# Kernel optimization log

Measured on AMD Instinct MI355X. Metric: run time of the kernel, lower is better.

## Reference

```python
import jax, jax.numpy as jnp
import numpy as np


def setup_inputs() -> dict:
    key = jax.random.key(0)
    k1, k2 = jax.random.split(key)
    quantum_state = jax.random.normal(k1, (8, 2048, 1024), dtype=jnp.float32)
    gate_params = jax.random.normal(k2, (3, 10, 4), dtype=jnp.float32)  # (n_layers, n_qubits, 4)
    return {"quantum_state": quantum_state, "gate_params": gate_params}


def _total_factor(gate_params):
    # gate.sum() = cos(a)e^{ib} + sin(a)e^{ig} - sin(a)e^{-ig} + cos(a)e^{-ib}
    #            = 2*cos(a)*cos(b) + 2j*sin(a)*sin(g)   (delta unused)
    a = gate_params[..., 0]
    b = gate_params[..., 1]
    g = gate_params[..., 2]
    re = 2.0 * jnp.cos(a) * jnp.cos(b)
    im = 2.0 * jnp.sin(a) * jnp.sin(g)
    s = jax.lax.complex(re, im).astype(jnp.complex64)  # (3, n_qubits)
    return jnp.prod(s)  # single complex scalar


def reference(quantum_state, gate_params):
    factor = _total_factor(gate_params)
    # torch: real state * complex scalar -> complex64 output
    return quantum_state.astype(jnp.complex64) * factor
```

## Files before the change

### kernel.cpp

```cpp
#include <hip/hip_runtime.h>


typedef float fvec4 __attribute__((ext_vector_type(4)));

__device__ __forceinline__ float2 wave_factor(const float* __restrict__ gp) {
    const int lane = threadIdx.x & 63;
    float re = 1.0f, im = 0.0f;
    if (lane < 30) {
        const float a = gp[lane * 4 + 0];
        const float b = gp[lane * 4 + 1];
        const float g = gp[lane * 4 + 2];
        re = 2.0f * cosf(a) * cosf(b);
        im = 2.0f * sinf(a) * sinf(g);
    }
    #pragma unroll
    for (int m = 1; m < 64; m <<= 1) {
        const float ore = __shfl_xor(re, m, 64);
        const float oim = __shfl_xor(im, m, 64);
        const float nre = re * ore - im * oim;
        const float nim = re * oim + im * ore;
        re = nre;
        im = nim;
    }
    return make_float2(re, im);
}

__global__ void __launch_bounds__(256) qp_real_kernel(const float* __restrict__ state,
                                                      const float* __restrict__ gp,
                                                      float* __restrict__ out,
                                                      long long n4 ) {
    const float fr = wave_factor(gp).x;
    const fvec4* __restrict__ in4 = reinterpret_cast<const fvec4*>(state);
    fvec4* __restrict__ out4 = reinterpret_cast<fvec4*>(out);
    const long long stride = (long long)gridDim.x * blockDim.x;
    for (long long i = (long long)blockIdx.x * blockDim.x + threadIdx.x; i < n4; i += stride) {
        fvec4 s = in4[i];
        fvec4 o = s * fr;
        __builtin_nontemporal_store(o, &out4[i]);
    }
}

__global__ void __launch_bounds__(256) qp_complex_kernel(const float* __restrict__ state,
                                                         const float* __restrict__ gp,
                                                         float* __restrict__ out,
                                                         long long n2 ) {
    const float2 f = wave_factor(gp);
    const float fr = f.x, fi = f.y;
    const float2* __restrict__ in2 = reinterpret_cast<const float2*>(state);
    fvec4* __restrict__ out4 = reinterpret_cast<fvec4*>(out);
    const long long stride = (long long)gridDim.x * blockDim.x;
    for (long long i = (long long)blockIdx.x * blockDim.x + threadIdx.x; i < n2; i += stride) {
        float2 s = in2[i];
        fvec4 o;
        o.x = s.x * fr;
        o.y = s.x * fi;
        o.z = s.y * fr;
        o.w = s.y * fi;
        __builtin_nontemporal_store(o, &out4[i]);
    }
}

extern "C" void kernel_launch(void* const* d_in, const int* in_sizes, int n_in,
                              void* d_out, int out_size, void* d_ws, size_t ws_size,
                              hipStream_t stream) {
    const float* state = (const float*)d_in[0];
    const float* gp = (const float*)d_in[1];
    float* out = (float*)d_out;

    const long long N = (long long)in_sizes[0];

    const int block = 256;
    const int grid = 4096;

    if ((long long)out_size == 2 * N) {
        qp_complex_kernel<<<grid, block, 0, stream>>>(state, gp, out, N / 2);
    } else {
        qp_real_kernel<<<grid, block, 0, stream>>>(state, gp, out, N / 4);
    }
}
```

Measured before the change: 25.83 us.

## Prefetch next state element, overlap factor computation with load, halve grid

Each kernel now issues its first state load before computing the gate factor, so memory latency overlaps the trig and shuffle reduction. The grid-stride loop is software-pipelined to load the next element before storing the current one. Fast __sinf/__cosf intrinsics replace the precise versions, nontemporal stores become regular stores, and the grid drops from 4096 to 2048 blocks. The fast intrinsics lower accuracy of the factor, and dropping nontemporal stores may change cache behaviour for the large output.

```diff
diff --git a/kernel.cpp b/kernel.cpp
--- a/kernel.cpp
+++ b/kernel.cpp
@@ -10,8 +10,8 @@
         const float a = gp[lane * 4 + 0];
         const float b = gp[lane * 4 + 1];
         const float g = gp[lane * 4 + 2];
-        re = 2.0f * cosf(a) * cosf(b);
-        im = 2.0f * sinf(a) * sinf(g);
+        re = 2.0f * __cosf(a) * __cosf(b);
+        im = 2.0f * __sinf(a) * __sinf(g);
     }
     #pragma unroll
     for (int m = 1; m < 64; m <<= 1) {
@@ -29,35 +29,55 @@
                                                       const float* __restrict__ gp,
                                                       float* __restrict__ out,
                                                       long long n4 ) {
-    const float fr = wave_factor(gp).x;
     const fvec4* __restrict__ in4 = reinterpret_cast<const fvec4*>(state);
     fvec4* __restrict__ out4 = reinterpret_cast<fvec4*>(out);
     const long long stride = (long long)gridDim.x * blockDim.x;
-    for (long long i = (long long)blockIdx.x * blockDim.x + threadIdx.x; i < n4; i += stride) {
-        fvec4 s = in4[i];
-        fvec4 o = s * fr;
-        __builtin_nontemporal_store(o, &out4[i]);
+    long long i = (long long)blockIdx.x * blockDim.x + threadIdx.x;
+    if (i >= n4) return;
+
+    fvec4 s = in4[i];
+    const float fr = wave_factor(gp).x;
+
+    while (i + stride < n4) {
+        fvec4 nxt = in4[i + stride];
+        out4[i] = s * fr;
+        s = nxt;
+        i += stride;
     }
+    out4[i] = s * fr;
 }
 
 __global__ void __launch_bounds__(256) qp_complex_kernel(const float* __restrict__ state,
                                                          const float* __restrict__ gp,
                                                          float* __restrict__ out,
                                                          long long n2 ) {
-    const float2 f = wave_factor(gp);
-    const float fr = f.x, fi = f.y;
     const float2* __restrict__ in2 = reinterpret_cast<const float2*>(state);
     fvec4* __restrict__ out4 = reinterpret_cast<fvec4*>(out);
     const long long stride = (long long)gridDim.x * blockDim.x;
-    for (long long i = (long long)blockIdx.x * blockDim.x + threadIdx.x; i < n2; i += stride) {
-        float2 s = in2[i];
+    long long i = (long long)blockIdx.x * blockDim.x + threadIdx.x;
+    if (i >= n2) return;
+
+    float2 s = in2[i];
+    const float2 f = wave_factor(gp);
+    const float fr = f.x, fi = f.y;
+
+    while (i + stride < n2) {
+        float2 nxt = in2[i + stride];
         fvec4 o;
         o.x = s.x * fr;
         o.y = s.x * fi;
         o.z = s.y * fr;
         o.w = s.y * fi;
-        __builtin_nontemporal_store(o, &out4[i]);
+        out4[i] = o;
+        s = nxt;
+        i += stride;
     }
+    fvec4 o;
+    o.x = s.x * fr;
+    o.y = s.x * fi;
+    o.z = s.y * fr;
+    o.w = s.y * fi;
+    out4[i] = o;
 }
 
 extern "C" void kernel_launch(void* const* d_in, const int* in_sizes, int n_in,
@@ -70,7 +90,7 @@
     const long long N = (long long)in_sizes[0];
 
     const int block = 256;
-    const int grid = 4096;
+    const int grid = 2048;
 
     if ((long long)out_size == 2 * N) {
         qp_complex_kernel<<<grid, block, 0, stream>>>(state, gp, out, N / 2);
```

Result: no change. 25.98 us (+0.6%).

## Launch one thread per element, drop grid-stride loop, use fast trig intrinsics

Applied to the files above, without the earlier changes.

Replaces the fixed 4096-block grid-stride loop with a grid sized to the data, so each thread processes a single element. The input load is issued before the factor reduction so the two can overlap. Trig calls are switched to the fast intrinsics and plain stores replace the nontemporal ones. The cost is that every thread recomputes the wave-level factor reduction once per element, and the fast intrinsics give slightly less accurate sine and cosine values.

```diff
diff --git a/kernel.cpp b/kernel.cpp
--- a/kernel.cpp
+++ b/kernel.cpp
@@ -10,8 +10,8 @@
         const float a = gp[lane * 4 + 0];
         const float b = gp[lane * 4 + 1];
         const float g = gp[lane * 4 + 2];
-        re = 2.0f * cosf(a) * cosf(b);
-        im = 2.0f * sinf(a) * sinf(g);
+        re = 2.0f * __cosf(a) * __cosf(b);
+        im = 2.0f * __sinf(a) * __sinf(g);
     }
     #pragma unroll
     for (int m = 1; m < 64; m <<= 1) {
@@ -29,35 +29,33 @@
                                                       const float* __restrict__ gp,
                                                       float* __restrict__ out,
                                                       long long n4 ) {
-    const float fr = wave_factor(gp).x;
+    const long long i = (long long)blockIdx.x * blockDim.x + threadIdx.x;
+    if (i >= n4) return;
     const fvec4* __restrict__ in4 = reinterpret_cast<const fvec4*>(state);
     fvec4* __restrict__ out4 = reinterpret_cast<fvec4*>(out);
-    const long long stride = (long long)gridDim.x * blockDim.x;
-    for (long long i = (long long)blockIdx.x * blockDim.x + threadIdx.x; i < n4; i += stride) {
-        fvec4 s = in4[i];
-        fvec4 o = s * fr;
-        __builtin_nontemporal_store(o, &out4[i]);
-    }
+
+    fvec4 s = in4[i];
+    const float fr = wave_factor(gp).x;
+    out4[i] = s * fr;
 }
 
 __global__ void __launch_bounds__(256) qp_complex_kernel(const float* __restrict__ state,
                                                          const float* __restrict__ gp,
                                                          float* __restrict__ out,
                                                          long long n2 ) {
-    const float2 f = wave_factor(gp);
-    const float fr = f.x, fi = f.y;
+    const long long i = (long long)blockIdx.x * blockDim.x + threadIdx.x;
+    if (i >= n2) return;
     const float2* __restrict__ in2 = reinterpret_cast<const float2*>(state);
     fvec4* __restrict__ out4 = reinterpret_cast<fvec4*>(out);
-    const long long stride = (long long)gridDim.x * blockDim.x;
-    for (long long i = (long long)blockIdx.x * blockDim.x + threadIdx.x; i < n2; i += stride) {
-        float2 s = in2[i];
-        fvec4 o;
-        o.x = s.x * fr;
-        o.y = s.x * fi;
-        o.z = s.y * fr;
-        o.w = s.y * fi;
-        __builtin_nontemporal_store(o, &out4[i]);
-    }
+
+    float2 s = in2[i];
+    const float2 f = wave_factor(gp);
+    fvec4 o;
+    o.x = s.x * f.x;
+    o.y = s.x * f.y;
+    o.z = s.y * f.x;
+    o.w = s.y * f.y;
+    out4[i] = o;
 }
 
 extern "C" void kernel_launch(void* const* d_in, const int* in_sizes, int n_in,
@@ -68,13 +66,15 @@
     float* out = (float*)d_out;
 
     const long long N = (long long)in_sizes[0];
-
     const int block = 256;
-    const int grid = 4096;
 
     if ((long long)out_size == 2 * N) {
-        qp_complex_kernel<<<grid, block, 0, stream>>>(state, gp, out, N / 2);
+        const long long n2 = N / 2;
+        const int grid = (int)((n2 + block - 1) / block);
+        qp_complex_kernel<<<grid, block, 0, stream>>>(state, gp, out, n2);
     } else {
-        qp_real_kernel<<<grid, block, 0, stream>>>(state, gp, out, N / 4);
+        const long long n4 = N / 4;
+        const int grid = (int)((n4 + block - 1) / block);
+        qp_real_kernel<<<grid, block, 0, stream>>>(state, gp, out, n4);
     }
 }
```

Measured after the change: 25.30 us. -2.1%, faster.
